# Optimization experiments

Measured on AMD Instinct MI355X. Metric: run time of the kernel, lower is better.

The kernel has to match this reference:

```python
import jax, jax.numpy as jnp
import numpy as np

B, L, D = 8, 2048, 64


def setup_inputs() -> dict:
    key = jax.random.key(0)
    kq, kk, kv = jax.random.split(key, 3)
    query = jax.random.normal(kq, (B, L, D), dtype=jnp.float32)
    key_t = jax.random.normal(kk, (B, L, D), dtype=jnp.float32)
    value = jax.random.normal(kv, (B, L, D), dtype=jnp.float32)
    return {"query": query, "key": key_t, "value": value}


def reference(query, key, value):
    d = query.shape[-1]
    # e = Q K^T / sqrt(d_k)   -> [B, Lq, Lk]
    scale = 1.0 / np.sqrt(float(d)).astype(np.float32)
    e = jnp.einsum("bqd,bkd->bqk", query, key) * scale
    # stable softmax over keys (matches exp(e - max)/sum in source)
    attention = jax.nn.softmax(e, axis=-1)
    # v = A V   -> [B, Lq, Dv]
    return jnp.einsum("bqk,bkd->bqd", attention, value)
```

## Files before the change

### kernel.cpp

```cpp
#include <hip/hip_runtime.h>


#define B_ 8
#define L_ 2048
#define D_ 64
#define NT 256

typedef _Float16 half8_t __attribute__((ext_vector_type(8)));
typedef _Float16 half4_t __attribute__((ext_vector_type(4)));
typedef float f32x4 __attribute__((ext_vector_type(4)));

#define SCALE_LOG2E 0.1803368801111244f

__global__ __launch_bounds__(NT) void prepass_frag(
    const float* __restrict__ K, const float* __restrict__ V,
    _Float16* __restrict__ K16F, _Float16* __restrict__ VT16F)
{
    const int blk = blockIdx.x;
    const int t = threadIdx.x;
    if (blk < 512) {
        const int b  = blk >> 6;
        const int kt = blk & 63;
        const int p    = t >> 6;
        const int lane = t & 63;
        const int quad = lane >> 4;
        const int l15  = lane & 15;
        const int s = p >> 1, c = p & 1;
        const int row = kt * 32 + s * 16 + l15;
        const float* kp = K + ((size_t)b * L_ + row) * D_ + c * 32 + quad * 8;
        const float4 f0 = *(const float4*)kp;
        const float4 f1 = *(const float4*)(kp + 4);
        half8_t w;
        w[0] = (_Float16)f0.x; w[1] = (_Float16)f0.y;
        w[2] = (_Float16)f0.z; w[3] = (_Float16)f0.w;
        w[4] = (_Float16)f1.x; w[5] = (_Float16)f1.y;
        w[6] = (_Float16)f1.z; w[7] = (_Float16)f1.w;
        *(half8_t*)&K16F[((size_t)(b * 64 + kt) * 4 + p) * 512 + lane * 8] = w;
    } else {
        const int vb = blk - 512;
        const int b  = vb >> 6;
        const int kt = vb & 63;
        #pragma unroll
        for (int i = 0; i < 2; ++i) {
            const int slot = i * NT + t;
            const int p    = slot >> 6;
            const int lane = slot & 63;
            const int quad = lane >> 4;
            const int l15  = lane & 15;
            const int d = p >> 1, ks = p & 1;
            const int row = kt * 32 + ks * 16 + quad * 4;
            const int col = d * 16 + l15;
            const float* vp = V + ((size_t)b * L_ + row) * D_ + col;
            half4_t a;
            a[0] = (_Float16)vp[0];
            a[1] = (_Float16)vp[D_];
            a[2] = (_Float16)vp[2 * D_];
            a[3] = (_Float16)vp[3 * D_];
            *(half4_t*)&VT16F[((size_t)(b * 64 + kt) * 8 + p) * 256 + lane * 4] = a;
        }
    }
}


#define LOADK(KT, BK)                                                           \
    {                                                                           \
        _Pragma("unroll") for (int s = 0; s < 2; ++s)                           \
        _Pragma("unroll") for (int c = 0; c < 2; ++c)                           \
            BK[s][c] = *(const half8_t*)&KbF[((size_t)(KT) * 4 + s * 2 + c) * 512 + lane * 8]; \
    }

#define PROC(KT, BK)                                                            \
    {                                                                           \
        half4_t av[4][2];                                                       \
        _Pragma("unroll") for (int d = 0; d < 4; ++d)                           \
        _Pragma("unroll") for (int ks = 0; ks < 2; ++ks)                        \
            av[d][ks] = *(const half4_t*)&VbF[((size_t)(KT) * 8 + d * 2 + ks) * 256 + lane * 4]; \
        f32x4 sc[2][2];                                                         \
        _Pragma("unroll") for (int ks = 0; ks < 2; ++ks)                        \
        _Pragma("unroll") for (int qs = 0; qs < 2; ++qs) {                      \
            f32x4 acc = (f32x4){0.f, 0.f, 0.f, 0.f};                            \
            acc = __builtin_amdgcn_mfma_f32_16x16x32_f16(BK[ks][0], bq[qs][0], acc, 0, 0, 0); \
            acc = __builtin_amdgcn_mfma_f32_16x16x32_f16(BK[ks][1], bq[qs][1], acc, 0, 0, 0); \
            sc[ks][qs] = acc;                                                   \
        }                                                                       \
        half4_t pb[2][2];                                                       \
        _Pragma("unroll") for (int ks = 0; ks < 2; ++ks)                        \
        _Pragma("unroll") for (int qs = 0; qs < 2; ++qs) {                      \
            const float p0 = __builtin_exp2f(sc[ks][qs][0]);                    \
            const float p1 = __builtin_exp2f(sc[ks][qs][1]);                    \
            const float p2 = __builtin_exp2f(sc[ks][qs][2]);                    \
            const float p3 = __builtin_exp2f(sc[ks][qs][3]);                    \
            lacc[qs] += (p0 + p1) + (p2 + p3);                                  \
            half4_t pv;                                                         \
            pv[0] = (_Float16)p0; pv[1] = (_Float16)p1;                         \
            pv[2] = (_Float16)p2; pv[3] = (_Float16)p3;                         \
            pb[ks][qs] = pv;                                                    \
        }                                                                       \
        _Pragma("unroll") for (int qs = 0; qs < 2; ++qs)                        \
        _Pragma("unroll") for (int d = 0; d < 4; ++d)                           \
        _Pragma("unroll") for (int ks = 0; ks < 2; ++ks)                        \
            ofr[qs][d] = __builtin_amdgcn_mfma_f32_16x16x16f16(av[d][ks], pb[ks][qs], ofr[qs][d], 0, 0, 0); \
    }

__global__ __launch_bounds__(512, 4) void attn_tlp(
    const float* __restrict__ Q,
    const _Float16* __restrict__ K16F,
    const _Float16* __restrict__ VT16F,
    float* __restrict__ O)
{
    __shared__ float Ored[512 * 17];
    __shared__ float Lred[256];

    const int t    = threadIdx.x;
    const int wave = t >> 6;
    const int lane = t & 63;
    const int quad = lane >> 4;
    const int l15  = lane & 15;

    const int b   = blockIdx.x & 7;
    const int qbi = blockIdx.x >> 3;
    const int qb  = qbi * 32;
    const int kt0 = wave * 8;

    const _Float16* KbF = K16F + (size_t)b * 64 * 4 * 512;
    const _Float16* VbF = VT16F + (size_t)b * 64 * 8 * 256;

    half8_t bq[2][2];
    #pragma unroll
    for (int qs = 0; qs < 2; ++qs) {
        const float* qp = Q + ((size_t)b * L_ + qb + qs * 16 + l15) * D_ + quad * 8;
        #pragma unroll
        for (int c = 0; c < 2; ++c) {
            const float4 f0 = *(const float4*)(qp + c * 32);
            const float4 f1 = *(const float4*)(qp + c * 32 + 4);
            bq[qs][c][0] = (_Float16)(f0.x * SCALE_LOG2E);
            bq[qs][c][1] = (_Float16)(f0.y * SCALE_LOG2E);
            bq[qs][c][2] = (_Float16)(f0.z * SCALE_LOG2E);
            bq[qs][c][3] = (_Float16)(f0.w * SCALE_LOG2E);
            bq[qs][c][4] = (_Float16)(f1.x * SCALE_LOG2E);
            bq[qs][c][5] = (_Float16)(f1.y * SCALE_LOG2E);
            bq[qs][c][6] = (_Float16)(f1.z * SCALE_LOG2E);
            bq[qs][c][7] = (_Float16)(f1.w * SCALE_LOG2E);
        }
    }

    f32x4 ofr[2][4];
    #pragma unroll
    for (int qs = 0; qs < 2; ++qs)
        #pragma unroll
        for (int d = 0; d < 4; ++d)
            ofr[qs][d] = (f32x4){0.f, 0.f, 0.f, 0.f};
    float lacc[2] = {0.f, 0.f};

    half8_t bkA[2][2], bkB[2][2];
    LOADK(kt0, bkA);
    for (int it = 0; it < 4; ++it) {
        const int kta = kt0 + it * 2;
        LOADK(kta + 1, bkB);
        PROC(kta, bkA);
        LOADK(kta + 2, bkA);
        PROC(kta + 1, bkB);
    }

    #pragma unroll
    for (int qs = 0; qs < 2; ++qs) {
        float v = lacc[qs];
        v += __shfl_xor(v, 16, 64);
        v += __shfl_xor(v, 32, 64);
        lacc[qs] = v;
    }
    if (quad == 0) {
        Lred[wave * 32 + l15] = lacc[0];
        Lred[wave * 32 + 16 + l15] = lacc[1];
    }

    #pragma unroll
    for (int qs = 0; qs < 2; ++qs) {
        __syncthreads();
        #pragma unroll
        for (int d = 0; d < 4; ++d)
            #pragma unroll
            for (int r = 0; r < 4; ++r)
                Ored[(wave * 64 + lane) * 17 + d * 4 + r] = ofr[qs][d][r];
        __syncthreads();
        if (wave < 4) {
            float lt = 0.f;
            #pragma unroll
            for (int w2 = 0; w2 < 8; ++w2)
                lt += Lred[w2 * 32 + qs * 16 + l15];
            const float inv = 1.0f / lt;
            f32x4 osum = (f32x4){0.f, 0.f, 0.f, 0.f};
            #pragma unroll
            for (int w2 = 0; w2 < 8; ++w2) {
                const float* src = &Ored[(w2 * 64 + lane) * 17 + wave * 4];
                osum[0] += src[0]; osum[1] += src[1];
                osum[2] += src[2]; osum[3] += src[3];
            }
            float4 outv;
            outv.x = osum[0] * inv; outv.y = osum[1] * inv;
            outv.z = osum[2] * inv; outv.w = osum[3] * inv;
            *(float4*)&O[((size_t)b * L_ + qb + qs * 16 + l15) * D_ + wave * 16 + quad * 4] = outv;
        }
    }
}

#define KS 72
__global__ __launch_bounds__(NT) void attn_mfma_f16(
    const float* __restrict__ Q, const float* __restrict__ K,
    const float* __restrict__ V, float* __restrict__ O)
{
    __shared__ __align__(16) _Float16 Kt[64 * KS];
    __shared__ __align__(16) _Float16 Vt[D_ * KS];
    __shared__ __align__(16) _Float16 Pt[4][16 * KS];

    const int t = threadIdx.x;
    const int wave = t >> 6, lane = t & 63, quad = lane >> 4, l15 = lane & 15;
    const int bpb = L_ / 64;
    const int b = blockIdx.x / bpb;
    const int qb = (blockIdx.x % bpb) * 64 + wave * 16;
    const size_t boff = (size_t)b * L_ * D_;

    half8_t aq[2];
    {
        const float* qp = Q + boff + (size_t)(qb + l15) * D_ + quad * 8;
        #pragma unroll
        for (int c = 0; c < 2; ++c) {
            const float4* p4 = (const float4*)(qp + c * 32);
            const float4 f0 = p4[0], f1 = p4[1];
            aq[c][0] = (_Float16)f0.x; aq[c][1] = (_Float16)f0.y;
            aq[c][2] = (_Float16)f0.z; aq[c][3] = (_Float16)f0.w;
            aq[c][4] = (_Float16)f1.x; aq[c][5] = (_Float16)f1.y;
            aq[c][6] = (_Float16)f1.z; aq[c][7] = (_Float16)f1.w;
        }
    }
    f32x4 ofr[4];
    #pragma unroll
    for (int d = 0; d < 4; ++d) ofr[d] = (f32x4){0.f, 0.f, 0.f, 0.f};
    float lacc[4] = {0.f, 0.f, 0.f, 0.f};
    const int skey = t & 63, sdg = t >> 6;
    _Float16* Pw = &Pt[wave][0];

    for (int kt = 0; kt < L_ / 64; ++kt) {
        __syncthreads();
        {
            const float4* kg4 = (const float4*)(K + boff + (size_t)(kt * 64 + skey) * D_ + sdg * 16);
            const float4 f0 = kg4[0], f1 = kg4[1], f2 = kg4[2], f3 = kg4[3];
            half8_t w0, w1;
            w0[0] = (_Float16)f0.x; w0[1] = (_Float16)f0.y;
            w0[2] = (_Float16)f0.z; w0[3] = (_Float16)f0.w;
            w0[4] = (_Float16)f1.x; w0[5] = (_Float16)f1.y;
            w0[6] = (_Float16)f1.z; w0[7] = (_Float16)f1.w;
            w1[0] = (_Float16)f2.x; w1[1] = (_Float16)f2.y;
            w1[2] = (_Float16)f2.z; w1[3] = (_Float16)f2.w;
            w1[4] = (_Float16)f3.x; w1[5] = (_Float16)f3.y;
            w1[6] = (_Float16)f3.z; w1[7] = (_Float16)f3.w;
            *(half8_t*)&Kt[skey * KS + sdg * 16] = w0;
            *(half8_t*)&Kt[skey * KS + sdg * 16 + 8] = w1;
        }
        {
            const float4* vg4 = (const float4*)(V + boff + (size_t)(kt * 64 + skey) * D_ + sdg * 16);
            #pragma unroll
            for (int i = 0; i < 4; ++i) {
                const float4 f = vg4[i];
                const int d0 = sdg * 16 + i * 4;
                Vt[(d0 + 0) * KS + skey] = (_Float16)f.x;
                Vt[(d0 + 1) * KS + skey] = (_Float16)f.y;
                Vt[(d0 + 2) * KS + skey] = (_Float16)f.z;
                Vt[(d0 + 3) * KS + skey] = (_Float16)f.w;
            }
        }
        __syncthreads();
        #pragma unroll
        for (int s = 0; s < 4; ++s) {
            const half8_t bk0 = *(const half8_t*)&Kt[(s * 16 + l15) * KS + quad * 8];
            const half8_t bk1 = *(const half8_t*)&Kt[(s * 16 + l15) * KS + 32 + quad * 8];
            f32x4 sc = (f32x4){0.f, 0.f, 0.f, 0.f};
            sc = __builtin_amdgcn_mfma_f32_16x16x32_f16(aq[0], bk0, sc, 0, 0, 0);
            sc = __builtin_amdgcn_mfma_f32_16x16x32_f16(aq[1], bk1, sc, 0, 0, 0);
            #pragma unroll
            for (int r = 0; r < 4; ++r) {
                const float p = __expf(sc[r] * 0.125f);
                lacc[r] += p;
                Pw[(quad * 4 + r) * KS + s * 16 + l15] = (_Float16)p;
            }
        }
        __syncthreads();
        #pragma unroll
        for (int c = 0; c < 2; ++c) {
            const half8_t ap = *(const half8_t*)&Pw[l15 * KS + c * 32 + quad * 8];
            #pragma unroll
            for (int d = 0; d < 4; ++d) {
                const half8_t bv = *(const half8_t*)&Vt[(d * 16 + l15) * KS + c * 32 + quad * 8];
                ofr[d] = __builtin_amdgcn_mfma_f32_16x16x32_f16(ap, bv, ofr[d], 0, 0, 0);
            }
        }
    }
    #pragma unroll
    for (int r = 0; r < 4; ++r) {
        float v = lacc[r];
        v += __shfl_xor(v, 1, 64);
        v += __shfl_xor(v, 2, 64);
        v += __shfl_xor(v, 4, 64);
        v += __shfl_xor(v, 8, 64);
        lacc[r] = v;
    }
    #pragma unroll
    for (int r = 0; r < 4; ++r) {
        const float inv = 1.0f / lacc[r];
        float* orow = O + boff + (size_t)(qb + quad * 4 + r) * D_ + l15;
        #pragma unroll
        for (int d = 0; d < 4; ++d) orow[d * 16] = ofr[d][r] * inv;
    }
}

extern "C" void kernel_launch(void* const* d_in, const int* in_sizes, int n_in,
                              void* d_out, int out_size, void* d_ws, size_t ws_size,
                              hipStream_t stream) {
    const float* Q = (const float*)d_in[0];
    const float* K = (const float*)d_in[1];
    const float* V = (const float*)d_in[2];
    float* O = (float*)d_out;

    if (ws_size >= (size_t)8 * 1024 * 1024) {
        _Float16* K16F  = (_Float16*)d_ws;
        _Float16* VT16F = K16F + (size_t)1048576;
        prepass_frag<<<1024, NT, 0, stream>>>(K, V, K16F, VT16F);
        attn_tlp<<<512, 512, 0, stream>>>(Q, K16F, VT16F, O);
    } else {
        attn_mfma_f16<<<256, NT, 0, stream>>>(Q, K, V, O);
    }
}
```

Before: 82.75 us.

## Fuse K/V fp16 prepass into attention via cooperative grid sync

Replaces the separate prepass kernel plus attention kernel with one cooperative kernel. Each block first converts its slice of K and V to the fp16 fragment layout, then calls a grid-wide barrier before running the same attention body. This removes one kernel launch and the gap between kernels, at the cost of a grid sync and the requirement that all 512 blocks are co-resident. If the cooperative launch fails, it falls back to the two-kernel path.

```diff
diff --git a/kernel.cpp b/kernel.cpp
--- a/kernel.cpp
+++ b/kernel.cpp
@@ -1,4 +1,7 @@
 #include <hip/hip_runtime.h>
+#include <hip/hip_cooperative_groups.h>
+
+namespace cg = cooperative_groups;
 
 
 #define B_ 8
@@ -11,56 +14,6 @@
 typedef float f32x4 __attribute__((ext_vector_type(4)));
 
 #define SCALE_LOG2E 0.1803368801111244f
-
-__global__ __launch_bounds__(NT) void prepass_frag(
-    const float* __restrict__ K, const float* __restrict__ V,
-    _Float16* __restrict__ K16F, _Float16* __restrict__ VT16F)
-{
-    const int blk = blockIdx.x;
-    const int t = threadIdx.x;
-    if (blk < 512) {
-        const int b  = blk >> 6;
-        const int kt = blk & 63;
-        const int p    = t >> 6;
-        const int lane = t & 63;
-        const int quad = lane >> 4;
-        const int l15  = lane & 15;
-        const int s = p >> 1, c = p & 1;
-        const int row = kt * 32 + s * 16 + l15;
-        const float* kp = K + ((size_t)b * L_ + row) * D_ + c * 32 + quad * 8;
-        const float4 f0 = *(const float4*)kp;
-        const float4 f1 = *(const float4*)(kp + 4);
-        half8_t w;
-        w[0] = (_Float16)f0.x; w[1] = (_Float16)f0.y;
-        w[2] = (_Float16)f0.z; w[3] = (_Float16)f0.w;
-        w[4] = (_Float16)f1.x; w[5] = (_Float16)f1.y;
-        w[6] = (_Float16)f1.z; w[7] = (_Float16)f1.w;
-        *(half8_t*)&K16F[((size_t)(b * 64 + kt) * 4 + p) * 512 + lane * 8] = w;
-    } else {
-        const int vb = blk - 512;
-        const int b  = vb >> 6;
-        const int kt = vb & 63;
-        #pragma unroll
-        for (int i = 0; i < 2; ++i) {
-            const int slot = i * NT + t;
-            const int p    = slot >> 6;
-            const int lane = slot & 63;
-            const int quad = lane >> 4;
-            const int l15  = lane & 15;
-            const int d = p >> 1, ks = p & 1;
-            const int row = kt * 32 + ks * 16 + quad * 4;
-            const int col = d * 16 + l15;
-            const float* vp = V + ((size_t)b * L_ + row) * D_ + col;
-            half4_t a;
-            a[0] = (_Float16)vp[0];
-            a[1] = (_Float16)vp[D_];
-            a[2] = (_Float16)vp[2 * D_];
-            a[3] = (_Float16)vp[3 * D_];
-            *(half4_t*)&VT16F[((size_t)(b * 64 + kt) * 8 + p) * 256 + lane * 4] = a;
-        }
-    }
-}
-
 
 #define LOADK(KT, BK)                                                           \
     {                                                                           \
@@ -102,6 +55,179 @@
             ofr[qs][d] = __builtin_amdgcn_mfma_f32_16x16x16f16(av[d][ks], pb[ks][qs], ofr[qs][d], 0, 0, 0); \
     }
 
+#define ATTN_BODY                                                               \
+    const _Float16* KbF = K16F + (size_t)b * 64 * 4 * 512;                      \
+    const _Float16* VbF = VT16F + (size_t)b * 64 * 8 * 256;                     \
+    half8_t bq[2][2];                                                           \
+    _Pragma("unroll") for (int qs = 0; qs < 2; ++qs) {                          \
+        const float* qp = Q + ((size_t)b * L_ + qb + qs * 16 + l15) * D_ + quad * 8; \
+        _Pragma("unroll") for (int c = 0; c < 2; ++c) {                         \
+            const float4 f0 = *(const float4*)(qp + c * 32);                    \
+            const float4 f1 = *(const float4*)(qp + c * 32 + 4);                \
+            bq[qs][c][0] = (_Float16)(f0.x * SCALE_LOG2E);                      \
+            bq[qs][c][1] = (_Float16)(f0.y * SCALE_LOG2E);                      \
+            bq[qs][c][2] = (_Float16)(f0.z * SCALE_LOG2E);                      \
+            bq[qs][c][3] = (_Float16)(f0.w * SCALE_LOG2E);                      \
+            bq[qs][c][4] = (_Float16)(f1.x * SCALE_LOG2E);                      \
+            bq[qs][c][5] = (_Float16)(f1.y * SCALE_LOG2E);                      \
+            bq[qs][c][6] = (_Float16)(f1.z * SCALE_LOG2E);                      \
+            bq[qs][c][7] = (_Float16)(f1.w * SCALE_LOG2E);                      \
+        }                                                                       \
+    }                                                                           \
+    f32x4 ofr[2][4];                                                            \
+    _Pragma("unroll") for (int qs = 0; qs < 2; ++qs)                            \
+        _Pragma("unroll") for (int d = 0; d < 4; ++d)                           \
+            ofr[qs][d] = (f32x4){0.f, 0.f, 0.f, 0.f};                           \
+    float lacc[2] = {0.f, 0.f};                                                 \
+    const int kt0 = wave * 8;                                                   \
+    half8_t bkA[2][2], bkB[2][2];                                               \
+    LOADK(kt0, bkA);                                                            \
+    for (int it = 0; it < 4; ++it) {                                            \
+        const int kta = kt0 + it * 2;                                           \
+        LOADK(kta + 1, bkB);                                                    \
+        PROC(kta, bkA);                                                         \
+        LOADK(kta + 2, bkA);                                                    \
+        PROC(kta + 1, bkB);                                                     \
+    }                                                                           \
+    _Pragma("unroll") for (int qs = 0; qs < 2; ++qs) {                          \
+        float v = lacc[qs];                                                     \
+        v += __shfl_xor(v, 16, 64);                                             \
+        v += __shfl_xor(v, 32, 64);                                             \
+        lacc[qs] = v;                                                           \
+    }                                                                           \
+    if (quad == 0) {                                                            \
+        Lred[wave * 32 + l15] = lacc[0];                                        \
+        Lred[wave * 32 + 16 + l15] = lacc[1];                                   \
+    }                                                                           \
+    _Pragma("unroll") for (int qs = 0; qs < 2; ++qs) {                          \
+        __syncthreads();                                                        \
+        _Pragma("unroll") for (int d = 0; d < 4; ++d)                           \
+            _Pragma("unroll") for (int r = 0; r < 4; ++r)                       \
+                Ored[(wave * 64 + lane) * 17 + d * 4 + r] = ofr[qs][d][r];      \
+        __syncthreads();                                                        \
+        if (wave < 4) {                                                         \
+            float lt = 0.f;                                                     \
+            _Pragma("unroll") for (int w2 = 0; w2 < 8; ++w2)                    \
+                lt += Lred[w2 * 32 + qs * 16 + l15];                            \
+            const float inv = 1.0f / lt;                                        \
+            f32x4 osum = (f32x4){0.f, 0.f, 0.f, 0.f};                           \
+            _Pragma("unroll") for (int w2 = 0; w2 < 8; ++w2) {                  \
+                const float* src = &Ored[(w2 * 64 + lane) * 17 + wave * 4];     \
+                osum[0] += src[0]; osum[1] += src[1];                           \
+                osum[2] += src[2]; osum[3] += src[3];                           \
+            }                                                                   \
+            float4 outv;                                                        \
+            outv.x = osum[0] * inv; outv.y = osum[1] * inv;                     \
+            outv.z = osum[2] * inv; outv.w = osum[3] * inv;                     \
+            *(float4*)&O[((size_t)b * L_ + qb + qs * 16 + l15) * D_ + wave * 16 + quad * 4] = outv; \
+        }                                                                       \
+    }
+
+__global__ __launch_bounds__(512, 4) void attn_coop(
+    const float* __restrict__ Q, const float* __restrict__ K,
+    const float* __restrict__ V,
+    _Float16* __restrict__ K16F, _Float16* __restrict__ VT16F,
+    float* __restrict__ O)
+{
+    __shared__ float Ored[512 * 17];
+    __shared__ float Lred[256];
+
+    const int t    = threadIdx.x;
+    const int wave = t >> 6;
+    const int lane = t & 63;
+    const int quad = lane >> 4;
+    const int l15  = lane & 15;
+
+    const int b   = blockIdx.x & 7;
+    const int qbi = blockIdx.x >> 3;
+    const int qb  = qbi * 32;
+    const int kt  = qbi;
+
+    if (wave < 4) {
+        const int p = wave;
+        const int s = p >> 1, c = p & 1;
+        const int row = kt * 32 + s * 16 + l15;
+        const float* kp = K + ((size_t)b * L_ + row) * D_ + c * 32 + quad * 8;
+        const float4 f0 = *(const float4*)kp;
+        const float4 f1 = *(const float4*)(kp + 4);
+        half8_t w;
+        w[0] = (_Float16)f0.x; w[1] = (_Float16)f0.y;
+        w[2] = (_Float16)f0.z; w[3] = (_Float16)f0.w;
+        w[4] = (_Float16)f1.x; w[5] = (_Float16)f1.y;
+        w[6] = (_Float16)f1.z; w[7] = (_Float16)f1.w;
+        *(half8_t*)&K16F[((size_t)(b * 64 + kt) * 4 + p) * 512 + lane * 8] = w;
+    } else {
+        #pragma unroll
+        for (int j = 0; j < 2; ++j) {
+            const int p = (wave - 4) * 2 + j;
+            const int d = p >> 1, ks = p & 1;
+            const int row = kt * 32 + ks * 16 + quad * 4;
+            const int col = d * 16 + l15;
+            const float* vp = V + ((size_t)b * L_ + row) * D_ + col;
+            half4_t a;
+            a[0] = (_Float16)vp[0];
+            a[1] = (_Float16)vp[D_];
+            a[2] = (_Float16)vp[2 * D_];
+            a[3] = (_Float16)vp[3 * D_];
+            *(half4_t*)&VT16F[((size_t)(b * 64 + kt) * 8 + p) * 256 + lane * 4] = a;
+        }
+    }
+
+    __threadfence();
+    cg::this_grid().sync();
+
+    ATTN_BODY
+}
+
+__global__ __launch_bounds__(NT) void prepass_frag(
+    const float* __restrict__ K, const float* __restrict__ V,
+    _Float16* __restrict__ K16F, _Float16* __restrict__ VT16F)
+{
+    const int blk = blockIdx.x;
+    const int t = threadIdx.x;
+    if (blk < 512) {
+        const int b  = blk >> 6;
+        const int kt = blk & 63;
+        const int p    = t >> 6;
+        const int lane = t & 63;
+        const int quad = lane >> 4;
+        const int l15  = lane & 15;
+        const int s = p >> 1, c = p & 1;
+        const int row = kt * 32 + s * 16 + l15;
+        const float* kp = K + ((size_t)b * L_ + row) * D_ + c * 32 + quad * 8;
+        const float4 f0 = *(const float4*)kp;
+        const float4 f1 = *(const float4*)(kp + 4);
+        half8_t w;
+        w[0] = (_Float16)f0.x; w[1] = (_Float16)f0.y;
+        w[2] = (_Float16)f0.z; w[3] = (_Float16)f0.w;
+        w[4] = (_Float16)f1.x; w[5] = (_Float16)f1.y;
+        w[6] = (_Float16)f1.z; w[7] = (_Float16)f1.w;
+        *(half8_t*)&K16F[((size_t)(b * 64 + kt) * 4 + p) * 512 + lane * 8] = w;
+    } else {
+        const int vb = blk - 512;
+        const int b  = vb >> 6;
+        const int kt = vb & 63;
+        #pragma unroll
+        for (int i = 0; i < 2; ++i) {
+            const int slot = i * NT + t;
+            const int p    = slot >> 6;
+            const int lane = slot & 63;
+            const int quad = lane >> 4;
+            const int l15  = lane & 15;
+            const int d = p >> 1, ks = p & 1;
+            const int row = kt * 32 + ks * 16 + quad * 4;
+            const int col = d * 16 + l15;
+            const float* vp = V + ((size_t)b * L_ + row) * D_ + col;
+            half4_t a;
+            a[0] = (_Float16)vp[0];
+            a[1] = (_Float16)vp[D_];
+            a[2] = (_Float16)vp[2 * D_];
+            a[3] = (_Float16)vp[3 * D_];
+            *(half4_t*)&VT16F[((size_t)(b * 64 + kt) * 8 + p) * 256 + lane * 4] = a;
+        }
+    }
+}
+
 __global__ __launch_bounds__(512, 4) void attn_tlp(
     const float* __restrict__ Q,
     const _Float16* __restrict__ K16F,
@@ -120,88 +246,8 @@
     const int b   = blockIdx.x & 7;
     const int qbi = blockIdx.x >> 3;
     const int qb  = qbi * 32;
-    const int kt0 = wave * 8;
-
-    const _Float16* KbF = K16F + (size_t)b * 64 * 4 * 512;
-    const _Float16* VbF = VT16F + (size_t)b * 64 * 8 * 256;
-
-    half8_t bq[2][2];
-    #pragma unroll
-    for (int qs = 0; qs < 2; ++qs) {
-        const float* qp = Q + ((size_t)b * L_ + qb + qs * 16 + l15) * D_ + quad * 8;
-        #pragma unroll
-        for (int c = 0; c < 2; ++c) {
-            const float4 f0 = *(const float4*)(qp + c * 32);
-            const float4 f1 = *(const float4*)(qp + c * 32 + 4);
-            bq[qs][c][0] = (_Float16)(f0.x * SCALE_LOG2E);
-            bq[qs][c][1] = (_Float16)(f0.y * SCALE_LOG2E);
-            bq[qs][c][2] = (_Float16)(f0.z * SCALE_LOG2E);
-            bq[qs][c][3] = (_Float16)(f0.w * SCALE_LOG2E);
-            bq[qs][c][4] = (_Float16)(f1.x * SCALE_LOG2E);
-            bq[qs][c][5] = (_Float16)(f1.y * SCALE_LOG2E);
-            bq[qs][c][6] = (_Float16)(f1.z * SCALE_LOG2E);
-            bq[qs][c][7] = (_Float16)(f1.w * SCALE_LOG2E);
-        }
-    }
-
-    f32x4 ofr[2][4];
-    #pragma unroll
-    for (int qs = 0; qs < 2; ++qs)
-        #pragma unroll
-        for (int d = 0; d < 4; ++d)
-            ofr[qs][d] = (f32x4){0.f, 0.f, 0.f, 0.f};
-    float lacc[2] = {0.f, 0.f};
-
-    half8_t bkA[2][2], bkB[2][2];
-    LOADK(kt0, bkA);
-    for (int it = 0; it < 4; ++it) {
-        const int kta = kt0 + it * 2;
-        LOADK(kta + 1, bkB);
-        PROC(kta, bkA);
-        LOADK(kta + 2, bkA);
-        PROC(kta + 1, bkB);
-    }
-
-    #pragma unroll
-    for (int qs = 0; qs < 2; ++qs) {
-        float v = lacc[qs];
-        v += __shfl_xor(v, 16, 64);
-        v += __shfl_xor(v, 32, 64);
-        lacc[qs] = v;
-    }
-    if (quad == 0) {
-        Lred[wave * 32 + l15] = lacc[0];
-        Lred[wave * 32 + 16 + l15] = lacc[1];
-    }
-
-    #pragma unroll
-    for (int qs = 0; qs < 2; ++qs) {
-        __syncthreads();
-        #pragma unroll
-        for (int d = 0; d < 4; ++d)
-            #pragma unroll
-            for (int r = 0; r < 4; ++r)
-                Ored[(wave * 64 + lane) * 17 + d * 4 + r] = ofr[qs][d][r];
-        __syncthreads();
-        if (wave < 4) {
-            float lt = 0.f;
-            #pragma unroll
-            for (int w2 = 0; w2 < 8; ++w2)
-                lt += Lred[w2 * 32 + qs * 16 + l15];
-            const float inv = 1.0f / lt;
-            f32x4 osum = (f32x4){0.f, 0.f, 0.f, 0.f};
-            #pragma unroll
-            for (int w2 = 0; w2 < 8; ++w2) {
-                const float* src = &Ored[(w2 * 64 + lane) * 17 + wave * 4];
-                osum[0] += src[0]; osum[1] += src[1];
-                osum[2] += src[2]; osum[3] += src[3];
-            }
-            float4 outv;
-            outv.x = osum[0] * inv; outv.y = osum[1] * inv;
-            outv.z = osum[2] * inv; outv.w = osum[3] * inv;
-            *(float4*)&O[((size_t)b * L_ + qb + qs * 16 + l15) * D_ + wave * 16 + quad * 4] = outv;
-        }
-    }
+
+    ATTN_BODY
 }
 
 #define KS 72
@@ -324,8 +370,15 @@
     if (ws_size >= (size_t)8 * 1024 * 1024) {
         _Float16* K16F  = (_Float16*)d_ws;
         _Float16* VT16F = K16F + (size_t)1048576;
-        prepass_frag<<<1024, NT, 0, stream>>>(K, V, K16F, VT16F);
-        attn_tlp<<<512, 512, 0, stream>>>(Q, K16F, VT16F, O);
+
+        void* args[] = { (void*)&Q, (void*)&K, (void*)&V,
+                         (void*)&K16F, (void*)&VT16F, (void*)&O };
+        hipError_t err = hipLaunchCooperativeKernel(
+            (void*)attn_coop, dim3(512), dim3(512), args, 0, stream);
+        if (err != hipSuccess) {
+            prepass_frag<<<1024, NT, 0, stream>>>(K, V, K16F, VT16F);
+            attn_tlp<<<512, 512, 0, stream>>>(Q, K16F, VT16F, O);
+        }
     } else {
         attn_mfma_f16<<<256, NT, 0, stream>>>(Q, K, V, O);
     }
```

Measured after the change: 239.0 us. 2.89x slower.
